# Kernel optimization log

Measured on AMD Instinct MI355X. Metric: run time of the kernel, lower is better.

Reference implementation:

```python
import jax, jax.numpy as jnp
import numpy as np

EPS_BN = 1e-5
EPS_LN = 1e-5
B_, CIN, COUT, H_, W_ = 8, 64, 128, 64, 64
DSTATE, DCONV, EXPAND = 16, 4, 2
DINNER = EXPAND * COUT            # 256
DTRANK = (COUT + 15) // 16        # 8


def setup_inputs() -> dict:
    key = jax.random.key(0)
    ks = jax.random.split(key, 24)
    g = lambda i, shape, s=0.02: jax.random.normal(ks[i], shape, jnp.float32) * s
    inp = {}
    inp["x"] = jax.random.normal(ks[0], (B_, CIN, H_, W_), jnp.float32)
    # conv-bn-relu x2
    inp["conv1_w"] = g(1, (COUT, CIN, 3, 3), 0.05)
    inp["conv1_b"] = jnp.zeros((COUT,), jnp.float32)
    inp["bn1_g"] = jnp.ones((COUT,), jnp.float32)
    inp["bn1_b"] = jnp.zeros((COUT,), jnp.float32)
    inp["bn1_m"] = g(2, (COUT,), 0.1)
    inp["bn1_v"] = jnp.ones((COUT,), jnp.float32)
    inp["conv2_w"] = g(3, (COUT, COUT, 3, 3), 0.05)
    inp["conv2_b"] = jnp.zeros((COUT,), jnp.float32)
    inp["bn2_g"] = jnp.ones((COUT,), jnp.float32)
    inp["bn2_b"] = jnp.zeros((COUT,), jnp.float32)
    inp["bn2_m"] = g(4, (COUT,), 0.1)
    inp["bn2_v"] = jnp.ones((COUT,), jnp.float32)
    # Mamba params (mamba_ssm defaults: projections bias-free except dt_proj)
    inp["in_proj_w"] = g(5, (2 * DINNER, COUT))
    inp["conv1d_w"] = g(6, (DINNER, 1, DCONV), 0.1)   # depthwise
    inp["conv1d_b"] = jnp.zeros((DINNER,), jnp.float32)
    inp["x_proj_w"] = g(7, (DTRANK + 2 * DSTATE, DINNER))
    inp["dt_proj_w"] = g(8, (DINNER, DTRANK), 0.1)
    inp["dt_proj_b"] = g(9, (DINNER,), 0.5)
    # S4D-real init: A = -[1..d_state] per channel
    A = jnp.tile(jnp.arange(1, DSTATE + 1, dtype=jnp.float32)[None, :], (DINNER, 1))
    inp["A_log"] = jnp.log(A)
    inp["D"] = jnp.ones((DINNER,), jnp.float32)
    inp["out_proj_w"] = g(10, (COUT, DINNER))
    inp["ln_g"] = jnp.ones((COUT,), jnp.float32)
    inp["ln_b"] = jnp.zeros((COUT,), jnp.float32)
    return inp


def _conv3x3(x, w, b):
    y = jax.lax.conv_general_dilated(x, w, (1, 1), ((1, 1), (1, 1)),
                                     dimension_numbers=("NCHW", "OIHW", "NCHW"))
    return y + b[None, :, None, None]


def _bn_eval(x, g, b, m, v):
    inv = jax.lax.rsqrt(v + EPS_BN)
    return (x - m[None, :, None, None]) * (g * inv)[None, :, None, None] + b[None, :, None, None]


def _mamba(x_flat, in_proj_w, conv1d_w, conv1d_b, x_proj_w, dt_proj_w, dt_proj_b, A_log, D, out_proj_w):
    # x_flat: (B, L, C)
    Bsz, L, _ = x_flat.shape
    xz = jnp.einsum("blc,ec->ble", x_flat, in_proj_w)          # (B, L, 2*di)
    xm, z = jnp.split(xz, 2, axis=-1)                           # each (B, L, di)
    # causal depthwise conv1d over time
    xt = jnp.transpose(xm, (0, 2, 1))                           # (B, di, L)
    xt = jax.lax.conv_general_dilated(xt, conv1d_w, (1,), ((DCONV - 1, 0),),
                                      dimension_numbers=("NCH", "OIH", "NCH"),
                                      feature_group_count=DINNER)
    xt = xt + conv1d_b[None, :, None]
    x_ssm = jax.nn.silu(jnp.transpose(xt, (0, 2, 1)))           # (B, L, di)
    xdb = jnp.einsum("bld,ed->ble", x_ssm, x_proj_w)            # (B, L, dt_rank+2*ds)
    dt_r = xdb[..., :DTRANK]
    Bm = xdb[..., DTRANK:DTRANK + DSTATE]                       # (B, L, ds)
    Cm = xdb[..., DTRANK + DSTATE:]                             # (B, L, ds)
    dt = jax.nn.softplus(jnp.einsum("blr,dr->bld", dt_r, dt_proj_w) + dt_proj_b)
    A = -jnp.exp(A_log)                                         # (di, ds)

    def step(h, inp):
        dt_t, B_t, C_t, x_t = inp                               # (B,di) (B,ds) (B,ds) (B,di)
        dA = jnp.exp(dt_t[:, :, None] * A)                      # (B, di, ds)
        h = dA * h + (dt_t * x_t)[:, :, None] * B_t[:, None, :]
        y = jnp.einsum("bds,bs->bd", h, C_t)
        return h, y

    xs = (jnp.swapaxes(dt, 0, 1), jnp.swapaxes(Bm, 0, 1),
          jnp.swapaxes(Cm, 0, 1), jnp.swapaxes(x_ssm, 0, 1))
    h0 = jnp.zeros((Bsz, DINNER, DSTATE), jnp.float32)
    _, ys = jax.lax.scan(step, h0, xs)                          # (L, B, di)
    y = jnp.swapaxes(ys, 0, 1) + D * x_ssm
    y = y * jax.nn.silu(z)
    return jnp.einsum("bld,od->blo", y, out_proj_w)             # (B, L, C)


def reference(x, conv1_w, conv1_b, bn1_g, bn1_b, bn1_m, bn1_v,
              conv2_w, conv2_b, bn2_g, bn2_b, bn2_m, bn2_v,
              in_proj_w, conv1d_w, conv1d_b, x_proj_w, dt_proj_w, dt_proj_b,
              A_log, D, out_proj_w, ln_g, ln_b):
    h = jax.nn.relu(_bn_eval(_conv3x3(x, conv1_w, conv1_b), bn1_g, bn1_b, bn1_m, bn1_v))
    h = jax.nn.relu(_bn_eval(_conv3x3(h, conv2_w, conv2_b), bn2_g, bn2_b, bn2_m, bn2_v))
    Bsz, C, Hh, Ww = h.shape
    seq = jnp.transpose(h, (0, 2, 3, 1)).reshape(Bsz, Hh * Ww, C)
    seq = _mamba(seq, in_proj_w, conv1d_w, conv1d_b, x_proj_w,
                 dt_proj_w, dt_proj_b, A_log, D, out_proj_w)
    # LayerNorm over channels
    mu = jnp.mean(seq, axis=-1, keepdims=True)
    var = jnp.mean(jnp.square(seq - mu), axis=-1, keepdims=True)
    seq = (seq - mu) * jax.lax.rsqrt(var + EPS_LN) * ln_g + ln_b
    return jnp.transpose(seq.reshape(Bsz, Hh, Ww, C), (0, 3, 1, 2))
```

## Files before the change

kernel.cpp:

```cpp
#include <hip/hip_runtime.h>
#include <hip/hip_bf16.h>


typedef __attribute__((ext_vector_type(8))) short bf16x8;
typedef __attribute__((ext_vector_type(4))) float f32x4;

#define DEV __device__ __forceinline__

constexpr float LOG2E = 1.44269504088896f;

DEV float siluf(float v) {
  return v * __builtin_amdgcn_rcpf(1.f + __expf(-v));
}

DEV unsigned short f2bf(float f) {
  __hip_bfloat16 h = __float2bfloat16(f);
  return *reinterpret_cast<unsigned short*>(&h);
}

DEV float bf2f(unsigned short u) {
  unsigned int x = (unsigned int)u << 16;
  return __builtin_bit_cast(float, x);
}

DEV void gll16(const void* g, void* l) {
  __builtin_amdgcn_global_load_lds(
      (const __attribute__((address_space(1))) void*)g,
      (__attribute__((address_space(3))) void*)l, 16, 0, 0);
}

constexpr int NC = 256;
constexpr int CL = 16;

DEV void zero_border(unsigned short* buf, int CI, int tid0, int nthreads) {
  for (int w = tid0; w < 8 * 260; w += nthreads) {
    int b = w / 260, e = w % 260;
    int y, x;
    if (e < 132) { y = (e < 66) ? 0 : 65; x = (e < 66) ? e : e - 66; }
    else { int e2 = e - 132; y = 1 + (e2 >> 1); x = (e2 & 1) ? 65 : 0; }
    uint4* p = reinterpret_cast<uint4*>(buf + ((size_t)((b * 66 + y) * 66 + x)) * CI);
    for (int k = 0; k < CI / 8; ++k) p[k] = uint4{0u, 0u, 0u, 0u};
  }
}

__global__ __launch_bounds__(256) void prologue(
    const float* __restrict__ X, unsigned short* __restrict__ Xb,
    const float* __restrict__ conv1_w, const float* __restrict__ conv2_w,
    const float* __restrict__ in_proj_w, const float* __restrict__ out_proj_w,
    const float* __restrict__ x_proj_w, const float* __restrict__ A_log,
    unsigned short* __restrict__ wb1, unsigned short* __restrict__ wb2,
    unsigned short* __restrict__ win, unsigned short* __restrict__ wout,
    unsigned short* __restrict__ xpwb, float* __restrict__ An2f,
    unsigned short* __restrict__ h1p)
{
  __shared__ float t[64][65];
  const int blk = blockIdx.x;
  const int tid = threadIdx.x;
  if (blk < 512) {
    const int b = blk >> 6, y = blk & 63;
    for (int i = tid; i < 4096; i += 256) {
      int c = i >> 6, xx = i & 63;
      t[c][xx] = X[(((size_t)b * 64 + c) * 64 + y) * 64 + xx];
    }
    __syncthreads();
    for (int i = tid; i < 4096; i += 256) {
      int xx = i >> 6, c = i & 63;
      Xb[(((size_t)(b * 66 + y + 1) * 66) + xx + 1) * 64 + c] = f2bf(t[c][xx]);
    }
  } else if (blk < 1904) {
    int idx = (blk - 512) * 256 + tid;
    if (idx < 73728) {
      int co = idx / 576, r = idx % 576, tp = r >> 6, ci = r & 63;
      wb1[idx] = f2bf(conv1_w[((size_t)co * 64 + ci) * 9 + tp]);
    } else if (idx < 221184) {
      int i = idx - 73728;
      int co = i / 1152, r = i % 1152, tp = r >> 7, ci = r & 127;
      wb2[i] = f2bf(conv2_w[((size_t)co * 128 + ci) * 9 + tp]);
    } else if (idx < 286720) {
      int i = idx - 221184; win[i] = f2bf(in_proj_w[i]);
    } else if (idx < 319488) {
      int i = idx - 286720; wout[i] = f2bf(out_proj_w[i]);
    } else if (idx < 352256) {
      int i = idx - 319488; int r = i >> 8, c = i & 255;
      xpwb[i] = (r < 40) ? f2bf(x_proj_w[r * 256 + c]) : (unsigned short)0;
    } else if (idx < 356352) {
      int i = idx - 352256;
      An2f[i] = -__expf(A_log[i]) * LOG2E;
    }
  } else {
    int tid0 = (blk - 1904) * 256 + tid;
    zero_border(Xb, 64, tid0, 16 * 256);
    zero_border(h1p, 128, tid0, 16 * 256);
  }
}

template<int CI, int PADOUT>
__global__ __launch_bounds__(512) void conv_mfma(
    const unsigned short* __restrict__ Xp,
    const unsigned short* __restrict__ Wb,
    const float* __restrict__ bc,
    const float* __restrict__ bg, const float* __restrict__ bb,
    const float* __restrict__ bm, const float* __restrict__ bv,
    unsigned short* __restrict__ Y)
{
  constexpr int KC  = 3 * CI / 64;
  constexpr int NCH = 3 * KC;
  __shared__ bf16x8 ldsA[2][512];

  const int tid  = threadIdx.x;
  const int lane = tid & 63;
  const int wid  = tid >> 6;
  const int n0 = wid * 16;
  const int y = blockIdx.x, b = blockIdx.y;
  const int lr = lane & 15, kq = lane >> 4, lk = kq * 8;

  auto stage = [&](int buf, int c) {
    const int dy = c / KC, kc = c - dy * KC;
    const unsigned short* g = Xp
        + (size_t)((b * 66 + y + dy) * 66) * CI
        + (size_t)lane * CI + kc * 64 + wid * 8;
    gll16(g, &ldsA[buf][wid * 64]);
  };

  f32x4 acc[4];
  #pragma unroll
  for (int i = 0; i < 4; ++i) acc[i] = f32x4{0.f, 0.f, 0.f, 0.f};

  stage(0, 0);
  __syncthreads();

  #pragma unroll
  for (int c = 0; c < NCH; ++c) {
    if (c + 1 < NCH) stage((c + 1) & 1, c + 1);
    const int dy = c / KC, kc = c - dy * KC;
    bf16x8 bw[2];
    #pragma unroll
    for (int t = 0; t < 2; ++t)
      bw[t] = *reinterpret_cast<const bf16x8*>(
          Wb + (size_t)(n0 + lr) * (9 * CI)
             + dy * 3 * CI + kc * 64 + t * 32 + lk);
    const bf16x8* Ab = ldsA[c & 1];
    #pragma unroll
    for (int t = 0; t < 2; ++t)
      #pragma unroll
      for (int mf = 0; mf < 4; ++mf) {
        bf16x8 afr = Ab[(t * 4 + kq) * 64 + mf * 16 + lr];
        acc[mf] = __builtin_amdgcn_mfma_f32_16x16x32_bf16(
            afr, bw[t], acc[mf], 0, 0, 0);
      }
    __syncthreads();
  }

  {
    int n = n0 + lr;
    float aS = bg[n] * rsqrtf(bv[n] + 1e-5f);
    float aB = (bc[n] - bm[n]) * aS + bb[n];
    #pragma unroll
    for (int mf = 0; mf < 4; ++mf)
      #pragma unroll
      for (int i = 0; i < 4; ++i) {
        int m = mf * 16 + kq * 4 + i;
        float v = fmaxf(acc[mf][i] * aS + aB, 0.f);
        if (PADOUT)
          Y[((size_t)(b * 66 + y + 1) * 66 + m + 1) * 128 + n] = f2bf(v);
        else
          Y[((size_t)(b * 4096 + y * 64 + m)) * 128 + n] = f2bf(v);
      }
  }
}

__global__ __launch_bounds__(256) void inproj_fused(
    const unsigned short* __restrict__ A,
    const unsigned short* __restrict__ Wn,
    const float* __restrict__ c1w,
    const float* __restrict__ c1b,
    unsigned short* __restrict__ xsu,
    unsigned short* __restrict__ zbu)
{
  constexpr int KDIM = 128;
  __shared__ bf16x8 ldsA[2][512];
  __shared__ unsigned short xmt[67][136];
  __shared__ unsigned short s3[3][128];
  __shared__ float cw[128][4];
  __shared__ float cbias[128];

  const int tid = threadIdx.x;
  const int lane = tid & 63, wid = tid >> 6;
  const int m0 = blockIdx.x * 64;
  const int by = blockIdx.y;
  const int n0 = by * 128 + wid * 32;
  const int lr = lane & 15, kq = lane >> 4, lk = kq * 8;
  const int l0 = m0 & 4095;

  if (by < 2) {
    for (int w = tid; w < 384; w += 256) {
      int j = w >> 7, k = w & 127;
      s3[j][k] = (l0 == 0) ? (unsigned short)0
                           : A[(size_t)(m0 - 3 + j) * 128 + k];
    }
    if (tid < 128) {
      int dd = by * 128 + tid;
      cw[tid][0] = c1w[dd * 4 + 0]; cw[tid][1] = c1w[dd * 4 + 1];
      cw[tid][2] = c1w[dd * 4 + 2]; cw[tid][3] = c1w[dd * 4 + 3];
      cbias[tid] = c1b[dd];
    }
  }

  bf16x8 bw[2][2][2];
  #pragma unroll
  for (int c = 0; c < 2; ++c)
    #pragma unroll
    for (int t = 0; t < 2; ++t)
      #pragma unroll
      for (int nf = 0; nf < 2; ++nf)
        bw[c][t][nf] = *reinterpret_cast<const bf16x8*>(
            Wn + (size_t)(n0 + nf * 16 + lr) * KDIM + c * 64 + t * 32 + lk);

  auto stage = [&](int buf, int c) {
    const unsigned short* g = A + (size_t)(m0 + lane) * KDIM + c * 64 + wid * 16;
    gll16(g,     &ldsA[buf][(wid * 2) * 64]);
    gll16(g + 8, &ldsA[buf][(wid * 2 + 1) * 64]);
  };

  f32x4 acc[4][2];
  #pragma unroll
  for (int i = 0; i < 4; ++i)
    #pragma unroll
    for (int j = 0; j < 2; ++j) acc[i][j] = f32x4{0.f, 0.f, 0.f, 0.f};

  stage(0, 0);
  __syncthreads();

  #pragma unroll
  for (int c = 0; c < 2; ++c) {
    if (c + 1 < 2) stage((c + 1) & 1, c + 1);
    const bf16x8* Ab = ldsA[c & 1];
    #pragma unroll
    for (int t = 0; t < 2; ++t)
      #pragma unroll
      for (int mf = 0; mf < 4; ++mf) {
        bf16x8 afr = Ab[(t * 4 + kq) * 64 + mf * 16 + lr];
        #pragma unroll
        for (int nf = 0; nf < 2; ++nf)
          acc[mf][nf] = __builtin_amdgcn_mfma_f32_16x16x32_bf16(
              afr, bw[c][t][nf], acc[mf][nf], 0, 0, 0);
      }
    __syncthreads();
  }

  if (by >= 2) {
    #pragma unroll
    for (int nf = 0; nf < 2; ++nf) {
      int n = n0 + nf * 16 + lr - 256;
      #pragma unroll
      for (int mf = 0; mf < 4; ++mf)
        #pragma unroll
        for (int i = 0; i < 4; ++i)
          zbu[(size_t)(m0 + mf * 16 + kq * 4 + i) * 256 + n] =
              f2bf(siluf(acc[mf][nf][i]));
    }
    return;
  }

  #pragma unroll
  for (int nf = 0; nf < 2; ++nf) {
    int ch = wid * 32 + nf * 16 + lr;
    #pragma unroll
    for (int mf = 0; mf < 4; ++mf)
      #pragma unroll
      for (int i = 0; i < 4; ++i)
        xmt[3 + mf * 16 + kq * 4 + i][ch] = f2bf(acc[mf][nf][i]);
  }
  __syncthreads();

  for (int w = tid; w < 384; w += 256) {
    int j = w >> 7, ch = w & 127;
    float a = 0.f;
    if (l0 != 0) {
      const unsigned short* wr = Wn + (size_t)(by * 128 + ch) * 128;
      #pragma unroll 4
      for (int k0 = 0; k0 < 128; k0 += 8) {
        bf16x8 wv = *reinterpret_cast<const bf16x8*>(wr + k0);
        #pragma unroll
        for (int k = 0; k < 8; ++k)
          a = fmaf(bf2f(s3[j][k0 + k]), bf2f((unsigned short)wv[k]), a);
      }
    }
    xmt[j][ch] = f2bf(a);
  }
  __syncthreads();

  const int tg = tid & 15, ch8 = tid >> 4;
  float wr8[8][4], br8[8];
  #pragma unroll
  for (int k = 0; k < 8; ++k) {
    int chl = ch8 * 8 + k;
    wr8[k][0] = cw[chl][0]; wr8[k][1] = cw[chl][1];
    wr8[k][2] = cw[chl][2]; wr8[k][3] = cw[chl][3];
    br8[k] = cbias[chl];
  }
  #pragma unroll
  for (int tk = 0; tk < 4; ++tk) {
    int m = tg * 4 + tk;
    float o[8];
    #pragma unroll
    for (int k = 0; k < 8; ++k) o[k] = br8[k];
    #pragma unroll
    for (int j = 0; j < 4; ++j) {
      uint4 xv = *reinterpret_cast<const uint4*>(&xmt[m + j][ch8 * 8]);
      const unsigned short* xs = reinterpret_cast<const unsigned short*>(&xv);
      #pragma unroll
      for (int k = 0; k < 8; ++k)
        o[k] = fmaf(bf2f(xs[k]), wr8[k][j], o[k]);
    }
    unsigned int pk[4];
    #pragma unroll
    for (int k = 0; k < 4; ++k) {
      unsigned short lo = f2bf(siluf(o[2 * k]));
      unsigned short hi = f2bf(siluf(o[2 * k + 1]));
      pk[k] = (unsigned int)lo | ((unsigned int)hi << 16);
    }
    *reinterpret_cast<uint4*>(
        &xsu[(size_t)(m0 + m) * 256 + by * 128 + ch8 * 8]) =
        *reinterpret_cast<uint4*>(pk);
  }
}

__global__ __launch_bounds__(256) void outproj_ln(
    const unsigned short* __restrict__ A,
    const unsigned short* __restrict__ Wn,
    const float* __restrict__ lg, const float* __restrict__ lb,
    float* __restrict__ out)
{
  constexpr int KDIM = 256;
  constexpr int NCH = KDIM / 64;
  __shared__ bf16x8 ldsA[2][512];
  __shared__ float buf[64][129];

  const int lane = threadIdx.x & 63;
  const int wid  = threadIdx.x >> 6;
  const int m0 = blockIdx.x * 64;
  const int n0 = wid * 32;
  const int lr = lane & 15, kq = lane >> 4, lk = kq * 8;

  bf16x8 bw[NCH][2][2];
  #pragma unroll
  for (int c = 0; c < NCH; ++c)
    #pragma unroll
    for (int t = 0; t < 2; ++t)
      #pragma unroll
      for (int nf = 0; nf < 2; ++nf)
        bw[c][t][nf] = *reinterpret_cast<const bf16x8*>(
            Wn + (size_t)(n0 + nf * 16 + lr) * KDIM + c * 64 + t * 32 + lk);

  auto stage = [&](int buf2, int c) {
    const unsigned short* g = A + (size_t)(m0 + lane) * KDIM + c * 64 + wid * 16;
    gll16(g,     &ldsA[buf2][(wid * 2) * 64]);
    gll16(g + 8, &ldsA[buf2][(wid * 2 + 1) * 64]);
  };

  f32x4 acc[4][2];
  #pragma unroll
  for (int i = 0; i < 4; ++i)
    #pragma unroll
    for (int j = 0; j < 2; ++j) acc[i][j] = f32x4{0.f, 0.f, 0.f, 0.f};

  stage(0, 0);
  __syncthreads();

  #pragma unroll
  for (int c = 0; c < NCH; ++c) {
    if (c + 1 < NCH) stage((c + 1) & 1, c + 1);
    const bf16x8* Ab = ldsA[c & 1];
    #pragma unroll
    for (int t = 0; t < 2; ++t)
      #pragma unroll
      for (int mf = 0; mf < 4; ++mf) {
        bf16x8 afr = Ab[(t * 4 + kq) * 64 + mf * 16 + lr];
        #pragma unroll
        for (int nf = 0; nf < 2; ++nf)
          acc[mf][nf] = __builtin_amdgcn_mfma_f32_16x16x32_bf16(
              afr, bw[c][t][nf], acc[mf][nf], 0, 0, 0);
      }
    __syncthreads();
  }

  #pragma unroll
  for (int nf = 0; nf < 2; ++nf) {
    int n = n0 + nf * 16 + lr;
    #pragma unroll
    for (int mf = 0; mf < 4; ++mf)
      #pragma unroll
      for (int i = 0; i < 4; ++i)
        buf[mf * 16 + kq * 4 + i][n] = acc[mf][nf][i];
  }
  __syncthreads();

  const int tid = threadIdx.x;
  const int tt = tid >> 2, q = tid & 3;
  float s = 0.f, sq = 0.f;
  #pragma unroll
  for (int i = 0; i < 32; ++i) {
    float v = buf[tt][q * 32 + i];
    s += v; sq += v * v;
  }
  s  += __shfl_xor(s, 1);  s  += __shfl_xor(s, 2);
  sq += __shfl_xor(sq, 1); sq += __shfl_xor(sq, 2);
  float mu = s * (1.f / 128.f);
  float var = sq * (1.f / 128.f) - mu * mu;
  float rstd = rsqrtf(fmaxf(var, 0.f) + 1e-5f);
  #pragma unroll
  for (int i = 0; i < 32; ++i) {
    int c = q * 32 + i;
    buf[tt][c] = (buf[tt][c] - mu) * rstd * lg[c] + lb[c];
  }
  __syncthreads();

  const int bb = m0 >> 12, l0 = m0 & 4095;
  for (int idx = tid; idx < 64 * 128; idx += 256) {
    int c = idx >> 6, t2 = idx & 63;
    out[((size_t)bb * 128 + c) * 4096 + l0 + t2] = buf[t2][c];
  }
}

__global__ __launch_bounds__(256) void scan_pass1(
    const unsigned short* __restrict__ xssm,
    const unsigned short* __restrict__ xpw,
    const float* __restrict__ dtw, const float* __restrict__ dtb,
    const float* __restrict__ An2f,
    unsigned short* __restrict__ Qb, float* __restrict__ S,
    float* __restrict__ xdb)
{
  __shared__ __align__(16) float sh[CL][40];
  const int c = blockIdx.x, b = blockIdx.y;
  const int d = threadIdx.x;
  const int lane = threadIdx.x & 63, wid = threadIdx.x >> 6;
  if (wid < 3) {
    const int col0 = wid * 16;
    const int plr = lane & 15, plk = (lane >> 4) * 8;
    f32x4 pacc = f32x4{0.f, 0.f, 0.f, 0.f};
    const unsigned short* Xrow =
        xssm + ((size_t)b * 4096 + (size_t)c * CL + plr) * 256;
    const unsigned short* Wrow = xpw + (size_t)(col0 + plr) * 256;
    #pragma unroll
    for (int k0 = 0; k0 < 256; k0 += 32) {
      bf16x8 af = *reinterpret_cast<const bf16x8*>(Xrow + k0 + plk);
      bf16x8 bf = *reinterpret_cast<const bf16x8*>(Wrow + k0 + plk);
      pacc = __builtin_amdgcn_mfma_f32_16x16x32_bf16(af, bf, pacc, 0, 0, 0);
    }
    int col = col0 + (lane & 15);
    if (col < 40) {
      #pragma unroll
      for (int i = 0; i < 4; ++i)
        sh[(lane >> 4) * 4 + i][col] = pacc[i];
    }
  }
  float4 w0 = *reinterpret_cast<const float4*>(&dtw[d * 8]);
  float4 w1 = *reinterpret_cast<const float4*>(&dtw[d * 8 + 4]);
  const float bdt = dtb[d];
  float An2[16], h[16];
  {
    const f32x4* a2 = reinterpret_cast<const f32x4*>(&An2f[d * 16]);
    #pragma unroll
    for (int q = 0; q < 4; ++q) {
      f32x4 v = a2[q];
      An2[q * 4 + 0] = v[0]; An2[q * 4 + 1] = v[1];
      An2[q * 4 + 2] = v[2]; An2[q * 4 + 3] = v[3];
    }
  }
  const float An2_0 = An2[0];
  bool usePow = true;
  #pragma unroll
  for (int s = 1; s < 16; ++s)
    usePow = usePow &&
        (fabsf(An2[s] - (float)(s + 1) * An2_0) <= 1e-4f * fabsf(An2[s]));
  #pragma unroll
  for (int s = 0; s < 16; ++s) h[s] = 0.f;
  __syncthreads();

  if (d < CL * 10) {
    reinterpret_cast<float4*>(&xdb[((size_t)b * 4096 + (size_t)c * CL) * 40])[d] =
        reinterpret_cast<const float4*>(&sh[0][0])[d];
  }

  float sdt = 0.f;
  const size_t xbase = ((size_t)b * 4096 + (size_t)c * CL) * 256 + d;
  unsigned short xu = xssm[xbase];
  for (int l = 0; l < CL; ++l) {
    unsigned short xun = (l + 1 < CL) ? xssm[xbase + (size_t)(l + 1) * 256]
                                      : (unsigned short)0;
    const float4* row = reinterpret_cast<const float4*>(sh[l]);
    float4 r0 = row[0], r1 = row[1];
    float acc = bdt;
    acc = fmaf(r0.x, w0.x, acc); acc = fmaf(r0.y, w0.y, acc);
    acc = fmaf(r0.z, w0.z, acc); acc = fmaf(r0.w, w0.w, acc);
    acc = fmaf(r1.x, w1.x, acc); acc = fmaf(r1.y, w1.y, acc);
    acc = fmaf(r1.z, w1.z, acc); acc = fmaf(r1.w, w1.w, acc);
    float dt = (acc > 20.f) ? acc : __logf(1.f + __expf(acc));
    sdt += dt;
    float dtx = dt * bf2f(xu);
    if (usePow) {
      float r1p = __builtin_amdgcn_exp2f(dt * An2_0);
      float r2 = r1p * r1p, r3 = r2 * r1p, r4 = r2 * r2;
      float pj[4] = {r1p, r2, r3, r4};
      float base = 1.f;
      #pragma unroll
      for (int q = 0; q < 4; ++q) {
        float4 Bq = row[2 + q];
        float bb4[4] = {Bq.x, Bq.y, Bq.z, Bq.w};
        #pragma unroll
        for (int j = 0; j < 4; ++j) {
          int s = q * 4 + j;
          h[s] = fmaf(base * pj[j], h[s], dtx * bb4[j]);
        }
        base *= r4;
      }
    } else {
      #pragma unroll
      for (int q = 0; q < 4; ++q) {
        float4 Bq = row[2 + q];
        float bb4[4] = {Bq.x, Bq.y, Bq.z, Bq.w};
        #pragma unroll
        for (int j = 0; j < 4; ++j) {
          int s = q * 4 + j;
          float dA = __builtin_amdgcn_exp2f(dt * An2[s]);
          h[s] = fmaf(dA, h[s], dtx * bb4[j]);
        }
      }
    }
    xu = xun;
  }
  unsigned int pk[8];
  #pragma unroll
  for (int k = 0; k < 8; ++k)
    pk[k] = (unsigned int)f2bf(h[2 * k]) | ((unsigned int)f2bf(h[2 * k + 1]) << 16);
  uint4* qp = reinterpret_cast<uint4*>(
      &Qb[(((size_t)b * NC + c) * 256 + d) * 16]);
  qp[0] = *reinterpret_cast<uint4*>(pk);
  qp[1] = *reinterpret_cast<uint4*>(pk + 4);
  S[((size_t)b * NC + c) * 256 + d] = sdt;
}

__global__ __launch_bounds__(256) void scan_combine(
    unsigned short* __restrict__ Qb, const float* __restrict__ S,
    const float* __restrict__ An2f)
{
  constexpr int TC = 64;
  __shared__ unsigned short qt[TC][256];
  __shared__ float mt[TC][256];
  const int b = blockIdx.x >> 4, dsg = blockIdx.x & 15;
  const int tid = threadIdx.x;
  const int ds = dsg * 256 + tid;
  const int d = ds >> 4;
  const float An2 = An2f[ds];
  float h = 0.f;
  for (int ct = 0; ct < NC; ct += TC) {
    #pragma unroll 8
    for (int r = 0; r < TC; ++r) {
      int c = ct + r;
      qt[r][tid] = Qb[(size_t)(b * NC + c) * 4096 + ds];
      mt[r][tid] = __builtin_amdgcn_exp2f(
          An2 * S[(size_t)(b * NC + c) * 256 + d]);
    }
    #pragma unroll 8
    for (int r = 0; r < TC; ++r) {
      float q = bf2f(qt[r][tid]);
      qt[r][tid] = f2bf(h);
      h = fmaf(mt[r][tid], h, q);
    }
    #pragma unroll 8
    for (int r = 0; r < TC; ++r)
      Qb[(size_t)(b * NC + ct + r) * 4096 + ds] = qt[r][tid];
  }
}

__global__ __launch_bounds__(256) void scan_pass2(
    const unsigned short* __restrict__ xssm,
    const float* __restrict__ xdb,
    const unsigned short* __restrict__ zb,
    const float* __restrict__ dtw, const float* __restrict__ dtb,
    const float* __restrict__ An2f, const float* __restrict__ Dp,
    const unsigned short* __restrict__ Hstart, unsigned short* __restrict__ ybf)
{
  __shared__ __align__(16) float sh[CL][40];
  const int c = blockIdx.x, b = blockIdx.y;
  const int d = threadIdx.x;
  if (d < CL * 10) {
    reinterpret_cast<float4*>(&sh[0][0])[d] =
        reinterpret_cast<const float4*>(
            &xdb[((size_t)b * 4096 + (size_t)c * CL) * 40])[d];
  }
  float4 w0 = *reinterpret_cast<const float4*>(&dtw[d * 8]);
  float4 w1 = *reinterpret_cast<const float4*>(&dtw[d * 8 + 4]);
  const float bdt = dtb[d];
  const float Dd = Dp[d];
  float An2[16], h[16];
  {
    const f32x4* a2 = reinterpret_cast<const f32x4*>(&An2f[d * 16]);
    #pragma unroll
    for (int q = 0; q < 4; ++q) {
      f32x4 v = a2[q];
      An2[q * 4 + 0] = v[0]; An2[q * 4 + 1] = v[1];
      An2[q * 4 + 2] = v[2]; An2[q * 4 + 3] = v[3];
    }
  }
  const float An2_0 = An2[0];
  bool usePow = true;
  #pragma unroll
  for (int s = 1; s < 16; ++s)
    usePow = usePow &&
        (fabsf(An2[s] - (float)(s + 1) * An2_0) <= 1e-4f * fabsf(An2[s]));
  {
    const uint4* hp = reinterpret_cast<const uint4*>(
        &Hstart[(((size_t)b * NC + c) * 256 + d) * 16]);
    uint4 h0 = hp[0], h1 = hp[1];
    const unsigned short* hs = reinterpret_cast<const unsigned short*>(&h0);
    #pragma unroll
    for (int s = 0; s < 8; ++s) h[s] = bf2f(hs[s]);
    const unsigned short* hs2 = reinterpret_cast<const unsigned short*>(&h1);
    #pragma unroll
    for (int s = 0; s < 8; ++s) h[8 + s] = bf2f(hs2[s]);
  }
  __syncthreads();

  const size_t xbase = ((size_t)b * 4096 + (size_t)c * CL) * 256 + d;
  unsigned short xu = xssm[xbase], zu = zb[xbase];
  for (int l = 0; l < CL; ++l) {
    unsigned short xun = 0, zun = 0;
    if (l + 1 < CL) {
      xun = xssm[xbase + (size_t)(l + 1) * 256];
      zun = zb[xbase + (size_t)(l + 1) * 256];
    }
    const float4* row = reinterpret_cast<const float4*>(sh[l]);
    float4 r0 = row[0], r1 = row[1];
    float acc = bdt;
    acc = fmaf(r0.x, w0.x, acc); acc = fmaf(r0.y, w0.y, acc);
    acc = fmaf(r0.z, w0.z, acc); acc = fmaf(r0.w, w0.w, acc);
    acc = fmaf(r1.x, w1.x, acc); acc = fmaf(r1.y, w1.y, acc);
    acc = fmaf(r1.z, w1.z, acc); acc = fmaf(r1.w, w1.w, acc);
    float dt = (acc > 20.f) ? acc : __logf(1.f + __expf(acc));
    float xv = bf2f(xu);
    float dtx = dt * xv;
    float yq[4] = {0.f, 0.f, 0.f, 0.f};
    if (usePow) {
      float r1p = __builtin_amdgcn_exp2f(dt * An2_0);
      float r2 = r1p * r1p, r3 = r2 * r1p, r4 = r2 * r2;
      float pj[4] = {r1p, r2, r3, r4};
      float base = 1.f;
      #pragma unroll
      for (int q = 0; q < 4; ++q) {
        float4 Bq = row[2 + q], Cq = row[6 + q];
        float bb4[4] = {Bq.x, Bq.y, Bq.z, Bq.w};
        float cc4[4] = {Cq.x, Cq.y, Cq.z, Cq.w};
        #pragma unroll
        for (int j = 0; j < 4; ++j) {
          int s = q * 4 + j;
          h[s] = fmaf(base * pj[j], h[s], dtx * bb4[j]);
          yq[q] = fmaf(h[s], cc4[j], yq[q]);
        }
        base *= r4;
      }
    } else {
      #pragma unroll
      for (int q = 0; q < 4; ++q) {
        float4 Bq = row[2 + q], Cq = row[6 + q];
        float bb4[4] = {Bq.x, Bq.y, Bq.z, Bq.w};
        float cc4[4] = {Cq.x, Cq.y, Cq.z, Cq.w};
        #pragma unroll
        for (int j = 0; j < 4; ++j) {
          int s = q * 4 + j;
          float dA = __builtin_amdgcn_exp2f(dt * An2[s]);
          h[s] = fmaf(dA, h[s], dtx * bb4[j]);
          yq[q] = fmaf(h[s], cc4[j], yq[q]);
        }
      }
    }
    float y = (yq[0] + yq[1]) + (yq[2] + yq[3]);
    y = (y + Dd * xv) * bf2f(zu);
    ybf[xbase + (size_t)l * 256] = f2bf(y);
    xu = xun; zu = zun;
  }
}

extern "C" void kernel_launch(void* const* d_in, const int* in_sizes, int n_in,
                              void* d_out, int out_size, void* d_ws, size_t ws_size,
                              hipStream_t stream) {
  const float* x        = (const float*)d_in[0];
  const float* conv1_w  = (const float*)d_in[1];
  const float* conv1_b  = (const float*)d_in[2];
  const float* bn1_g    = (const float*)d_in[3];
  const float* bn1_b    = (const float*)d_in[4];
  const float* bn1_m    = (const float*)d_in[5];
  const float* bn1_v    = (const float*)d_in[6];
  const float* conv2_w  = (const float*)d_in[7];
  const float* conv2_b  = (const float*)d_in[8];
  const float* bn2_g    = (const float*)d_in[9];
  const float* bn2_b    = (const float*)d_in[10];
  const float* bn2_m    = (const float*)d_in[11];
  const float* bn2_v    = (const float*)d_in[12];
  const float* in_proj_w  = (const float*)d_in[13];
  const float* conv1d_w   = (const float*)d_in[14];
  const float* conv1d_b   = (const float*)d_in[15];
  const float* x_proj_w   = (const float*)d_in[16];
  const float* dt_proj_w  = (const float*)d_in[17];
  const float* dt_proj_b  = (const float*)d_in[18];
  const float* A_log      = (const float*)d_in[19];
  const float* Dp         = (const float*)d_in[20];
  const float* out_proj_w = (const float*)d_in[21];
  const float* ln_g       = (const float*)d_in[22];
  const float* ln_b       = (const float*)d_in[23];
  float* out = (float*)d_out;

  float* ws_f = (float*)d_ws;
  unsigned short* xbp  = (unsigned short*)ws_f;
  unsigned short* ybf  = (unsigned short*)ws_f;
  float*          xdb  = ws_f + 4194304;
  float*          Sbuf = ws_f + 5505024;
  unsigned short* zbu  = (unsigned short*)(ws_f + 8388608);
  unsigned short* xsu  = (unsigned short*)(ws_f + 12582912);
  unsigned short* h1p  = (unsigned short*)(ws_f + 16777216);
  unsigned short* seqb = (unsigned short*)(ws_f + 19007488);
  unsigned short* Qb   = (unsigned short*)(ws_f + 16777216);
  unsigned short* wb1  = (unsigned short*)(ws_f + 25165824);
  unsigned short* wb2  = (unsigned short*)(ws_f + 25202688);
  unsigned short* win  = (unsigned short*)(ws_f + 25276416);
  unsigned short* wout = (unsigned short*)(ws_f + 25309184);
  unsigned short* xpwb = (unsigned short*)(ws_f + 25325568);
  float*          An2f = ws_f + 25341952;

  prologue<<<1920, 256, 0, stream>>>(
      x, xbp, conv1_w, conv2_w, in_proj_w, out_proj_w, x_proj_w, A_log,
      wb1, wb2, win, wout, xpwb, An2f, h1p);

  conv_mfma<64, 1><<<dim3(64, 8), 512, 0, stream>>>(
      xbp, wb1, conv1_b, bn1_g, bn1_b, bn1_m, bn1_v, h1p);
  conv_mfma<128, 0><<<dim3(64, 8), 512, 0, stream>>>(
      h1p, wb2, conv2_b, bn2_g, bn2_b, bn2_m, bn2_v, seqb);

  inproj_fused<<<dim3(512, 4), 256, 0, stream>>>(
      seqb, win, conv1d_w, conv1d_b, xsu, zbu);

  scan_pass1<<<dim3(NC, 8), 256, 0, stream>>>(
      xsu, xpwb, dt_proj_w, dt_proj_b, An2f, Qb, Sbuf, xdb);
  scan_combine<<<128, 256, 0, stream>>>(Qb, Sbuf, An2f);
  scan_pass2<<<dim3(NC, 8), 256, 0, stream>>>(
      xsu, xdb, zbu, dt_proj_w, dt_proj_b, An2f, Dp, Qb, ybf);

  outproj_ln<<<512, 256, 0, stream>>>(ybf, wout, ln_g, ln_b, out);
}
```

Before: 191.3 us.

## Fuse scan second pass with out-projection and LayerNorm in one kernel

Merges scan_pass2 and outproj_ln into a single 512-thread kernel. Each block covers four scan chunks (64 timesteps) and each half of the block runs two chunks one after the other. The gated scan output is written as bf16 into shared memory and multiplied there by the out-projection weights with MFMA, then LayerNorm is applied and the result is written transposed to the output. This removes the global write and read of the intermediate y tensor and one kernel launch. In exchange, each thread's serial scan work doubles, there are fewer blocks, and shared memory per block goes up.

New measurement: 183.1 us. 1.04x faster.

```diff
diff --git a/kernel.cpp b/kernel.cpp
--- a/kernel.cpp
+++ b/kernel.cpp
@@ -323,103 +323,6 @@
     *reinterpret_cast<uint4*>(
         &xsu[(size_t)(m0 + m) * 256 + by * 128 + ch8 * 8]) =
         *reinterpret_cast<uint4*>(pk);
-  }
-}
-
-__global__ __launch_bounds__(256) void outproj_ln(
-    const unsigned short* __restrict__ A,
-    const unsigned short* __restrict__ Wn,
-    const float* __restrict__ lg, const float* __restrict__ lb,
-    float* __restrict__ out)
-{
-  constexpr int KDIM = 256;
-  constexpr int NCH = KDIM / 64;
-  __shared__ bf16x8 ldsA[2][512];
-  __shared__ float buf[64][129];
-
-  const int lane = threadIdx.x & 63;
-  const int wid  = threadIdx.x >> 6;
-  const int m0 = blockIdx.x * 64;
-  const int n0 = wid * 32;
-  const int lr = lane & 15, kq = lane >> 4, lk = kq * 8;
-
-  bf16x8 bw[NCH][2][2];
-  #pragma unroll
-  for (int c = 0; c < NCH; ++c)
-    #pragma unroll
-    for (int t = 0; t < 2; ++t)
-      #pragma unroll
-      for (int nf = 0; nf < 2; ++nf)
-        bw[c][t][nf] = *reinterpret_cast<const bf16x8*>(
-            Wn + (size_t)(n0 + nf * 16 + lr) * KDIM + c * 64 + t * 32 + lk);
-
-  auto stage = [&](int buf2, int c) {
-    const unsigned short* g = A + (size_t)(m0 + lane) * KDIM + c * 64 + wid * 16;
-    gll16(g,     &ldsA[buf2][(wid * 2) * 64]);
-    gll16(g + 8, &ldsA[buf2][(wid * 2 + 1) * 64]);
-  };
-
-  f32x4 acc[4][2];
-  #pragma unroll
-  for (int i = 0; i < 4; ++i)
-    #pragma unroll
-    for (int j = 0; j < 2; ++j) acc[i][j] = f32x4{0.f, 0.f, 0.f, 0.f};
-
-  stage(0, 0);
-  __syncthreads();
-
-  #pragma unroll
-  for (int c = 0; c < NCH; ++c) {
-    if (c + 1 < NCH) stage((c + 1) & 1, c + 1);
-    const bf16x8* Ab = ldsA[c & 1];
-    #pragma unroll
-    for (int t = 0; t < 2; ++t)
-      #pragma unroll
-      for (int mf = 0; mf < 4; ++mf) {
-        bf16x8 afr = Ab[(t * 4 + kq) * 64 + mf * 16 + lr];
-        #pragma unroll
-        for (int nf = 0; nf < 2; ++nf)
-          acc[mf][nf] = __builtin_amdgcn_mfma_f32_16x16x32_bf16(
-              afr, bw[c][t][nf], acc[mf][nf], 0, 0, 0);
-      }
-    __syncthreads();
-  }
-
-  #pragma unroll
-  for (int nf = 0; nf < 2; ++nf) {
-    int n = n0 + nf * 16 + lr;
-    #pragma unroll
-    for (int mf = 0; mf < 4; ++mf)
-      #pragma unroll
-      for (int i = 0; i < 4; ++i)
-        buf[mf * 16 + kq * 4 + i][n] = acc[mf][nf][i];
-  }
-  __syncthreads();
-
-  const int tid = threadIdx.x;
-  const int tt = tid >> 2, q = tid & 3;
-  float s = 0.f, sq = 0.f;
-  #pragma unroll
-  for (int i = 0; i < 32; ++i) {
-    float v = buf[tt][q * 32 + i];
-    s += v; sq += v * v;
-  }
-  s  += __shfl_xor(s, 1);  s  += __shfl_xor(s, 2);
-  sq += __shfl_xor(sq, 1); sq += __shfl_xor(sq, 2);
-  float mu = s * (1.f / 128.f);
-  float var = sq * (1.f / 128.f) - mu * mu;
-  float rstd = rsqrtf(fmaxf(var, 0.f) + 1e-5f);
-  #pragma unroll
-  for (int i = 0; i < 32; ++i) {
-    int c = q * 32 + i;
-    buf[tt][c] = (buf[tt][c] - mu) * rstd * lg[c] + lb[c];
-  }
-  __syncthreads();
-
-  const int bb = m0 >> 12, l0 = m0 & 4095;
-  for (int idx = tid; idx < 64 * 128; idx += 256) {
-    int c = idx >> 6, t2 = idx & 63;
-    out[((size_t)bb * 128 + c) * 4096 + l0 + t2] = buf[t2][c];
   }
 }
 
@@ -574,27 +477,41 @@
   }
 }
 
-__global__ __launch_bounds__(256) void scan_pass2(
+__global__ __launch_bounds__(512) void scan_pass2_fused(
     const unsigned short* __restrict__ xssm,
     const float* __restrict__ xdb,
     const unsigned short* __restrict__ zb,
     const float* __restrict__ dtw, const float* __restrict__ dtb,
     const float* __restrict__ An2f, const float* __restrict__ Dp,
-    const unsigned short* __restrict__ Hstart, unsigned short* __restrict__ ybf)
+    const unsigned short* __restrict__ Hstart,
+    const unsigned short* __restrict__ Wn,
+    const float* __restrict__ lg, const float* __restrict__ lb,
+    float* __restrict__ out)
 {
-  __shared__ __align__(16) float sh[CL][40];
-  const int c = blockIdx.x, b = blockIdx.y;
-  const int d = threadIdx.x;
-  if (d < CL * 10) {
-    reinterpret_cast<float4*>(&sh[0][0])[d] =
+  __shared__ __align__(16) float sh[4][CL][40];
+  __shared__ __align__(16) char yb_raw[64 * 264 * 2];
+  unsigned short (*ybuf)[264] =
+      reinterpret_cast<unsigned short(*)[264]>(yb_raw);
+  float (*buf)[132] = reinterpret_cast<float(*)[132]>(yb_raw);
+
+  const int cg = blockIdx.x, b = blockIdx.y;
+  const int c0 = cg * 4;
+  const int tid = threadIdx.x;
+  const int lane = tid & 63, wid = tid >> 6;
+  const int d = tid & 255;
+  const int half = tid >> 8;
+
+  for (int i = tid; i < 4 * CL * 10; i += 512) {
+    reinterpret_cast<float4*>(&sh[0][0][0])[i] =
         reinterpret_cast<const float4*>(
-            &xdb[((size_t)b * 4096 + (size_t)c * CL) * 40])[d];
-  }
+            &xdb[((size_t)b * 4096 + (size_t)c0 * CL) * 40])[i];
+  }
+
   float4 w0 = *reinterpret_cast<const float4*>(&dtw[d * 8]);
   float4 w1 = *reinterpret_cast<const float4*>(&dtw[d * 8 + 4]);
   const float bdt = dtb[d];
   const float Dd = Dp[d];
-  float An2[16], h[16];
+  float An2[16];
   {
     const f32x4* a2 = reinterpret_cast<const f32x4*>(&An2f[d * 16]);
     #pragma unroll
@@ -610,75 +527,147 @@
   for (int s = 1; s < 16; ++s)
     usePow = usePow &&
         (fabsf(An2[s] - (float)(s + 1) * An2_0) <= 1e-4f * fabsf(An2[s]));
+  __syncthreads();
+
+  for (int chh = 0; chh < 2; ++chh) {
+    const int ch = half * 2 + chh;
+    const int c = c0 + ch;
+    float h[16];
+    {
+      const uint4* hp = reinterpret_cast<const uint4*>(
+          &Hstart[(((size_t)b * NC + c) * 256 + d) * 16]);
+      uint4 h0 = hp[0], h1 = hp[1];
+      const unsigned short* hs = reinterpret_cast<const unsigned short*>(&h0);
+      #pragma unroll
+      for (int s = 0; s < 8; ++s) h[s] = bf2f(hs[s]);
+      const unsigned short* hs2 = reinterpret_cast<const unsigned short*>(&h1);
+      #pragma unroll
+      for (int s = 0; s < 8; ++s) h[8 + s] = bf2f(hs2[s]);
+    }
+    const size_t xbase = ((size_t)b * 4096 + (size_t)c * CL) * 256 + d;
+    unsigned short xu = xssm[xbase], zu = zb[xbase];
+    for (int l = 0; l < CL; ++l) {
+      unsigned short xun = 0, zun = 0;
+      if (l + 1 < CL) {
+        xun = xssm[xbase + (size_t)(l + 1) * 256];
+        zun = zb[xbase + (size_t)(l + 1) * 256];
+      }
+      const float4* row = reinterpret_cast<const float4*>(sh[ch][l]);
+      float4 r0 = row[0], r1 = row[1];
+      float acc = bdt;
+      acc = fmaf(r0.x, w0.x, acc); acc = fmaf(r0.y, w0.y, acc);
+      acc = fmaf(r0.z, w0.z, acc); acc = fmaf(r0.w, w0.w, acc);
+      acc = fmaf(r1.x, w1.x, acc); acc = fmaf(r1.y, w1.y, acc);
+      acc = fmaf(r1.z, w1.z, acc); acc = fmaf(r1.w, w1.w, acc);
+      float dt = (acc > 20.f) ? acc : __logf(1.f + __expf(acc));
+      float xv = bf2f(xu);
+      float dtx = dt * xv;
+      float yq[4] = {0.f, 0.f, 0.f, 0.f};
+      if (usePow) {
+        float r1p = __builtin_amdgcn_exp2f(dt * An2_0);
+        float r2 = r1p * r1p, r3 = r2 * r1p, r4 = r2 * r2;
+        float pj[4] = {r1p, r2, r3, r4};
+        float base = 1.f;
+        #pragma unroll
+        for (int q = 0; q < 4; ++q) {
+          float4 Bq = row[2 + q], Cq = row[6 + q];
+          float bb4[4] = {Bq.x, Bq.y, Bq.z, Bq.w};
+          float cc4[4] = {Cq.x, Cq.y, Cq.z, Cq.w};
+          #pragma unroll
+          for (int j = 0; j < 4; ++j) {
+            int s = q * 4 + j;
+            h[s] = fmaf(base * pj[j], h[s], dtx * bb4[j]);
+            yq[q] = fmaf(h[s], cc4[j], yq[q]);
+          }
+          base *= r4;
+        }
+      } else {
+        #pragma unroll
+        for (int q = 0; q < 4; ++q) {
+          float4 Bq = row[2 + q], Cq = row[6 + q];
+          float bb4[4] = {Bq.x, Bq.y, Bq.z, Bq.w};
+          float cc4[4] = {Cq.x, Cq.y, Cq.z, Cq.w};
+          #pragma unroll
+          for (int j = 0; j < 4; ++j) {
+            int s = q * 4 + j;
+            float dA = __builtin_amdgcn_exp2f(dt * An2[s]);
+            h[s] = fmaf(dA, h[s], dtx * bb4[j]);
+            yq[q] = fmaf(h[s], cc4[j], yq[q]);
+          }
+        }
+      }
+      float y = (yq[0] + yq[1]) + (yq[2] + yq[3]);
+      y = (y + Dd * xv) * bf2f(zu);
+      ybuf[ch * CL + l][d] = f2bf(y);
+      xu = xun; zu = zun;
+    }
+  }
+  __syncthreads();
+
+  const int n0g = wid * 16;
+  const int lr = lane & 15, kq = lane >> 4, lk = kq * 8;
+  bf16x8 bwv[4][2];
+  #pragma unroll
+  for (int c = 0; c < 4; ++c)
+    #pragma unroll
+    for (int t = 0; t < 2; ++t)
+      bwv[c][t] = *reinterpret_cast<const bf16x8*>(
+          Wn + (size_t)(n0g + lr) * 256 + c * 64 + t * 32 + lk);
+
+  f32x4 acc[4];
+  #pragma unroll
+  for (int i = 0; i < 4; ++i) acc[i] = f32x4{0.f, 0.f, 0.f, 0.f};
+  #pragma unroll
+  for (int c = 0; c < 4; ++c)
+    #pragma unroll
+    for (int t = 0; t < 2; ++t) {
+      const int kc = c * 64 + t * 32 + lk;
+      #pragma unroll
+      for (int mf = 0; mf < 4; ++mf) {
+        bf16x8 afr = *reinterpret_cast<const bf16x8*>(
+            &ybuf[mf * 16 + (t * 4 + kq) * 0 + lr][kc]);
+        afr = *reinterpret_cast<const bf16x8*>(&ybuf[mf * 16 + lr][kc]);
+        acc[mf] = __builtin_amdgcn_mfma_f32_16x16x32_bf16(
+            afr, bwv[c][t], acc[mf], 0, 0, 0);
+      }
+    }
+  __syncthreads();
+
   {
-    const uint4* hp = reinterpret_cast<const uint4*>(
-        &Hstart[(((size_t)b * NC + c) * 256 + d) * 16]);
-    uint4 h0 = hp[0], h1 = hp[1];
-    const unsigned short* hs = reinterpret_cast<const unsigned short*>(&h0);
-    #pragma unroll
-    for (int s = 0; s < 8; ++s) h[s] = bf2f(hs[s]);
-    const unsigned short* hs2 = reinterpret_cast<const unsigned short*>(&h1);
-    #pragma unroll
-    for (int s = 0; s < 8; ++s) h[8 + s] = bf2f(hs2[s]);
-  }
-  __syncthreads();
-
-  const size_t xbase = ((size_t)b * 4096 + (size_t)c * CL) * 256 + d;
-  unsigned short xu = xssm[xbase], zu = zb[xbase];
-  for (int l = 0; l < CL; ++l) {
-    unsigned short xun = 0, zun = 0;
-    if (l + 1 < CL) {
-      xun = xssm[xbase + (size_t)(l + 1) * 256];
-      zun = zb[xbase + (size_t)(l + 1) * 256];
-    }
-    const float4* row = reinterpret_cast<const float4*>(sh[l]);
-    float4 r0 = row[0], r1 = row[1];
-    float acc = bdt;
-    acc = fmaf(r0.x, w0.x, acc); acc = fmaf(r0.y, w0.y, acc);
-    acc = fmaf(r0.z, w0.z, acc); acc = fmaf(r0.w, w0.w, acc);
-    acc = fmaf(r1.x, w1.x, acc); acc = fmaf(r1.y, w1.y, acc);
-    acc = fmaf(r1.z, w1.z, acc); acc = fmaf(r1.w, w1.w, acc);
-    float dt = (acc > 20.f) ? acc : __logf(1.f + __expf(acc));
-    float xv = bf2f(xu);
-    float dtx = dt * xv;
-    float yq[4] = {0.f, 0.f, 0.f, 0.f};
-    if (usePow) {
-      float r1p = __builtin_amdgcn_exp2f(dt * An2_0);
-      float r2 = r1p * r1p, r3 = r2 * r1p, r4 = r2 * r2;
-      float pj[4] = {r1p, r2, r3, r4};
-      float base = 1.f;
-      #pragma unroll
-      for (int q = 0; q < 4; ++q) {
-        float4 Bq = row[2 + q], Cq = row[6 + q];
-        float bb4[4] = {Bq.x, Bq.y, Bq.z, Bq.w};
-        float cc4[4] = {Cq.x, Cq.y, Cq.z, Cq.w};
-        #pragma unroll
-        for (int j = 0; j < 4; ++j) {
-          int s = q * 4 + j;
-          h[s] = fmaf(base * pj[j], h[s], dtx * bb4[j]);
-          yq[q] = fmaf(h[s], cc4[j], yq[q]);
-        }
-        base *= r4;
-      }
-    } else {
-      #pragma unroll
-      for (int q = 0; q < 4; ++q) {
-        float4 Bq = row[2 + q], Cq = row[6 + q];
-        float bb4[4] = {Bq.x, Bq.y, Bq.z, Bq.w};
-        float cc4[4] = {Cq.x, Cq.y, Cq.z, Cq.w};
-        #pragma unroll
-        for (int j = 0; j < 4; ++j) {
-          int s = q * 4 + j;
-          float dA = __builtin_amdgcn_exp2f(dt * An2[s]);
-          h[s] = fmaf(dA, h[s], dtx * bb4[j]);
-          yq[q] = fmaf(h[s], cc4[j], yq[q]);
-        }
-      }
-    }
-    float y = (yq[0] + yq[1]) + (yq[2] + yq[3]);
-    y = (y + Dd * xv) * bf2f(zu);
-    ybf[xbase + (size_t)l * 256] = f2bf(y);
-    xu = xun; zu = zun;
+    int n = n0g + lr;
+    #pragma unroll
+    for (int mf = 0; mf < 4; ++mf)
+      #pragma unroll
+      for (int i = 0; i < 4; ++i)
+        buf[mf * 16 + kq * 4 + i][n] = acc[mf][i];
+  }
+  __syncthreads();
+
+  {
+    const int tt = tid >> 3, q = tid & 7;
+    float s = 0.f, sq = 0.f;
+    #pragma unroll
+    for (int i = 0; i < 16; ++i) {
+      float v = buf[tt][q * 16 + i];
+      s += v; sq += v * v;
+    }
+    s  += __shfl_xor(s, 1);  s  += __shfl_xor(s, 2);  s  += __shfl_xor(s, 4);
+    sq += __shfl_xor(sq, 1); sq += __shfl_xor(sq, 2); sq += __shfl_xor(sq, 4);
+    float mu = s * (1.f / 128.f);
+    float var = sq * (1.f / 128.f) - mu * mu;
+    float rstd = rsqrtf(fmaxf(var, 0.f) + 1e-5f);
+    #pragma unroll
+    for (int i = 0; i < 16; ++i) {
+      int ch = q * 16 + i;
+      buf[tt][ch] = (buf[tt][ch] - mu) * rstd * lg[ch] + lb[ch];
+    }
+  }
+  __syncthreads();
+
+  const int l0 = cg * 64;
+  for (int idx = tid; idx < 64 * 128; idx += 512) {
+    int ch = idx >> 6, t2 = idx & 63;
+    out[((size_t)b * 128 + ch) * 4096 + l0 + t2] = buf[t2][ch];
   }
 }
 
@@ -713,7 +702,6 @@
 
   float* ws_f = (float*)d_ws;
   unsigned short* xbp  = (unsigned short*)ws_f;
-  unsigned short* ybf  = (unsigned short*)ws_f;
   float*          xdb  = ws_f + 4194304;
   float*          Sbuf = ws_f + 5505024;
   unsigned short* zbu  = (unsigned short*)(ws_f + 8388608);
@@ -743,8 +731,7 @@
   scan_pass1<<<dim3(NC, 8), 256, 0, stream>>>(
       xsu, xpwb, dt_proj_w, dt_proj_b, An2f, Qb, Sbuf, xdb);
   scan_combine<<<128, 256, 0, stream>>>(Qb, Sbuf, An2f);
-  scan_pass2<<<dim3(NC, 8), 256, 0, stream>>>(
-      xsu, xdb, zbu, dt_proj_w, dt_proj_b, An2f, Dp, Qb, ybf);
-
-  outproj_ln<<<512, 256, 0, stream>>>(ybf, wout, ln_g, ln_b, out);
-}
+  scan_pass2_fused<<<dim3(64, 8), 512, 0, stream>>>(
+      xsu, xdb, zbu, dt_proj_w, dt_proj_b, An2f, Dp, Qb,
+      wout, ln_g, ln_b, out);
+}
```
